# Kernel tuning notes

Measured on AMD Instinct MI355X. Metric: run time of the kernel, lower is better.

Reference implementation:

```python
import jax, jax.numpy as jnp
import numpy as np

K_SIZE = 11  # fixed kernel size in the original module
HALF = K_SIZE // 2  # 5


def setup_inputs() -> dict:
    key = jax.random.key(0)
    N = 16777216  # 2**24 signal length
    inp = jax.random.normal(key, (N,), dtype=jnp.float32)
    scale = jnp.float32(1.0)  # learned scalar parameter (init arg s)
    return {"input": inp, "scale": scale}


def reference(input, scale):
    # Parabolic structuring element: h[k] = -z_k^2 / (4*scale), z_k = -5..5
    z = jnp.linspace(-HALF, HALF, K_SIZE, dtype=jnp.float32)
    h = -(z * z) / (4.0 * scale)  # [11]
    N = input.shape[0]
    # Pad with -inf so boundary windows truncate exactly like the banded matrix.
    padded = jnp.pad(input, (HALF, HALF), constant_values=-jnp.inf)
    # out[i] = max_k padded[i + k] + h[k]  (windowed max-plus / morphological dilation)
    acc = padded[0:N] + h[0]
    for k in range(1, K_SIZE):  # small fixed loop over 11 kernel taps
        acc = jnp.maximum(acc, padded[k:k + N] + h[k])
    return acc
```

## Files before the change

### kernel.cpp

```cpp
#include <hip/hip_runtime.h>
#include <math.h>

#define K_SIZE 11
#define HALF 5
#define BLOCK 256
#define EPT 8
#define TILE (BLOCK*EPT)

__global__ __launch_bounds__(BLOCK) void dilation1d_kernel(
    const float* __restrict__ in, const float* __restrict__ scale_p,
    float* __restrict__ out, int N)
{
    const float inv4s = 1.0f / (4.0f * scale_p[0]);

    const int t = threadIdx.x;
    const int g0 = blockIdx.x * TILE;
    const int base = g0 + t * EPT;
    const int lbase = base - 8;

    float r[24];
    const bool interior = (blockIdx.x != 0) && (blockIdx.x != gridDim.x - 1);
    if (interior) {
        const float4* p = (const float4*)(in + lbase);
        #pragma unroll
        for (int v = 0; v < 6; ++v) {
            float4 f = p[v];
            r[v*4+0] = f.x; r[v*4+1] = f.y; r[v*4+2] = f.z; r[v*4+3] = f.w;
        }
    } else {
        #pragma unroll
        for (int j = 0; j < 24; ++j) {
            int idx = lbase + j;
            r[j] = (idx >= 0 && idx < N) ? in[idx] : -INFINITY;
        }
    }

    float o[EPT];
    #pragma unroll
    for (int u = 0; u < EPT; ++u) {
        float m = -INFINITY;
        #pragma unroll
        for (int k = 0; k < K_SIZE; ++k) {
            const float zk = (float)(k - HALF);
            const float h = -(zk * zk) * inv4s;
            m = fmaxf(m, r[u + k + 3] + h);
        }
        o[u] = m;
    }

    float4* po = (float4*)(out + base);
    po[0] = make_float4(o[0], o[1], o[2], o[3]);
    po[1] = make_float4(o[4], o[5], o[6], o[7]);
}

extern "C" void kernel_launch(void* const* d_in, const int* in_sizes, int n_in,
                              void* d_out, int out_size, void* d_ws, size_t ws_size,
                              hipStream_t stream) {
    const float* in      = (const float*)d_in[0];
    const float* scale_p = (const float*)d_in[1];
    float* out           = (float*)d_out;
    const int N = in_sizes[0];
    const int grid = (N + TILE - 1) / TILE;
    hipLaunchKernelGGL(dilation1d_kernel, dim3(grid), dim3(BLOCK), 0, stream,
                       in, scale_p, out, N);
}
```

Before: 26.60 us.

## Use grid-stride tiles, symmetric tap pairing, and nontemporal output stores

Switches the launch to a fixed grid of at most 2048 blocks that loop over tiles in grid-stride fashion. The tap loop is rewritten to use the symmetry of the parabolic kernel: each symmetric pair is maxed first and a single offset added, which removes about half the adds. Output goes through nontemporal stores, and a guarded tail path is added for partial tiles. The point is to cut launch and tail overhead and ALU work on a memory-bound kernel. In exchange there is less parallelism per launch and possible changes in cache behaviour.

```diff
diff --git a/kernel.cpp b/kernel.cpp
--- a/kernel.cpp
+++ b/kernel.cpp
@@ -6,51 +6,63 @@
 #define BLOCK 256
 #define EPT 8
 #define TILE (BLOCK*EPT)
+#define GRID 2048
+
+typedef float floatx4 __attribute__((ext_vector_type(4)));
 
 __global__ __launch_bounds__(BLOCK) void dilation1d_kernel(
     const float* __restrict__ in, const float* __restrict__ scale_p,
     float* __restrict__ out, int N)
 {
     const float inv4s = 1.0f / (4.0f * scale_p[0]);
+    float h[HALF + 1];
+    #pragma unroll
+    for (int d = 0; d <= HALF; ++d) h[d] = -(float)(d * d) * inv4s;
 
-    const int t = threadIdx.x;
-    const int g0 = blockIdx.x * TILE;
-    const int base = g0 + t * EPT;
-    const int lbase = base - 8;
+    const int ntiles = (N + TILE - 1) / TILE;
+    for (int tile = blockIdx.x; tile < ntiles; tile += gridDim.x) {
+        const int base  = tile * TILE + threadIdx.x * EPT;
+        const int lbase = base - 8;
+        const bool interior = (tile != 0) && (tile != ntiles - 1);
 
-    float r[24];
-    const bool interior = (blockIdx.x != 0) && (blockIdx.x != gridDim.x - 1);
-    if (interior) {
-        const float4* p = (const float4*)(in + lbase);
+        float r[24];
+        if (interior) {
+            const floatx4* p = (const floatx4*)(in + lbase);
+            #pragma unroll
+            for (int v = 0; v < 6; ++v) {
+                floatx4 f = p[v];
+                r[v*4+0] = f.x; r[v*4+1] = f.y; r[v*4+2] = f.z; r[v*4+3] = f.w;
+            }
+        } else {
+            #pragma unroll
+            for (int j = 0; j < 24; ++j) {
+                int idx = lbase + j;
+                r[j] = (idx >= 0 && idx < N) ? in[idx] : -INFINITY;
+            }
+        }
+
+        float o[EPT];
         #pragma unroll
-        for (int v = 0; v < 6; ++v) {
-            float4 f = p[v];
-            r[v*4+0] = f.x; r[v*4+1] = f.y; r[v*4+2] = f.z; r[v*4+3] = f.w;
+        for (int u = 0; u < EPT; ++u) {
+            float m = r[u + 8];
+            #pragma unroll
+            for (int d = 1; d <= HALF; ++d)
+                m = fmaxf(m, fmaxf(r[u + 8 - d], r[u + 8 + d]) + h[d]);
+            o[u] = m;
         }
-    } else {
-        #pragma unroll
-        for (int j = 0; j < 24; ++j) {
-            int idx = lbase + j;
-            r[j] = (idx >= 0 && idx < N) ? in[idx] : -INFINITY;
+
+        if (interior || base + EPT <= N) {
+            floatx4* po = (floatx4*)(out + base);
+            floatx4 v0 = {o[0], o[1], o[2], o[3]};
+            floatx4 v1 = {o[4], o[5], o[6], o[7]};
+            __builtin_nontemporal_store(v0, po);
+            __builtin_nontemporal_store(v1, po + 1);
+        } else {
+            #pragma unroll
+            for (int u = 0; u < EPT; ++u)
+                if (base + u < N) out[base + u] = o[u];
         }
     }
-
-    float o[EPT];
-    #pragma unroll
-    for (int u = 0; u < EPT; ++u) {
-        float m = -INFINITY;
-        #pragma unroll
-        for (int k = 0; k < K_SIZE; ++k) {
-            const float zk = (float)(k - HALF);
-            const float h = -(zk * zk) * inv4s;
-            m = fmaxf(m, r[u + k + 3] + h);
-        }
-        o[u] = m;
-    }
-
-    float4* po = (float4*)(out + base);
-    po[0] = make_float4(o[0], o[1], o[2], o[3]);
-    po[1] = make_float4(o[4], o[5], o[6], o[7]);
 }
 
 extern "C" void kernel_launch(void* const* d_in, const int* in_sizes, int n_in,
@@ -60,7 +72,8 @@
     const float* scale_p = (const float*)d_in[1];
     float* out           = (float*)d_out;
     const int N = in_sizes[0];
-    const int grid = (N + TILE - 1) / TILE;
+    const int ntiles = (N + TILE - 1) / TILE;
+    const int grid = ntiles < GRID ? ntiles : GRID;
     hipLaunchKernelGGL(dilation1d_kernel, dim3(grid), dim3(BLOCK), 0, stream,
                        in, scale_p, out, N);
 }
```

Measured after the change: 28.42 us. 6.9% more time.

## Stage input tile with halo in LDS and exploit symmetric parabolic weights

Applied to the files above, without the earlier changes.

Each block now loads its 2048-element tile plus halo into shared memory with coalesced scalar loads, then each thread reads 20-element windows from LDS for two groups of 4 outputs. This replaces the overlapping per-thread global float4 loads, which fetched 24 values to produce 8 outputs. The tap loop uses the symmetry h[-d]=h[d] to take the max of the pair before adding, which reduces adds. It adds a __syncthreads and LDS traffic, and the global loads become scalar with bounds checks.

```diff
diff --git a/kernel.cpp b/kernel.cpp
--- a/kernel.cpp
+++ b/kernel.cpp
@@ -1,56 +1,70 @@
 #include <hip/hip_runtime.h>
 #include <math.h>
 
-#define K_SIZE 11
 #define HALF 5
 #define BLOCK 256
-#define EPT 8
-#define TILE (BLOCK*EPT)
+#define TILE 2048
+#define SLDS (TILE + 16)
+
+typedef float floatx4 __attribute__((ext_vector_type(4)));
 
 __global__ __launch_bounds__(BLOCK) void dilation1d_kernel(
     const float* __restrict__ in, const float* __restrict__ scale_p,
     float* __restrict__ out, int N)
 {
+    __shared__ float s[SLDS];
     const float inv4s = 1.0f / (4.0f * scale_p[0]);
+    float h[HALF + 1];
+    #pragma unroll
+    for (int d = 0; d <= HALF; ++d) h[d] = -(float)(d * d) * inv4s;
 
-    const int t = threadIdx.x;
+    const int t  = threadIdx.x;
     const int g0 = blockIdx.x * TILE;
-    const int base = g0 + t * EPT;
-    const int lbase = base - 8;
 
-    float r[24];
-    const bool interior = (blockIdx.x != 0) && (blockIdx.x != gridDim.x - 1);
-    if (interior) {
-        const float4* p = (const float4*)(in + lbase);
-        #pragma unroll
-        for (int v = 0; v < 6; ++v) {
-            float4 f = p[v];
-            r[v*4+0] = f.x; r[v*4+1] = f.y; r[v*4+2] = f.z; r[v*4+3] = f.w;
-        }
-    } else {
-        #pragma unroll
-        for (int j = 0; j < 24; ++j) {
-            int idx = lbase + j;
-            r[j] = (idx >= 0 && idx < N) ? in[idx] : -INFINITY;
+    #pragma unroll
+    for (int k = 0; k < 8; ++k) {
+        const int j = t + k * BLOCK;
+        const int idx = g0 - 8 + j;
+        s[j] = ((unsigned)idx < (unsigned)N) ? in[idx] : -INFINITY;
+    }
+    {
+        const int j = t + 8 * BLOCK;
+        if (j < SLDS) {
+            const int idx = g0 - 8 + j;
+            s[j] = ((unsigned)idx < (unsigned)N) ? in[idx] : -INFINITY;
         }
     }
+    __syncthreads();
 
-    float o[EPT];
     #pragma unroll
-    for (int u = 0; u < EPT; ++u) {
-        float m = -INFINITY;
+    for (int grp = 0; grp < 2; ++grp) {
+        const int p = 4 * t + grp * (TILE / 2);
+        float w[20];
+        const floatx4* ps = (const floatx4*)(s + p);
         #pragma unroll
-        for (int k = 0; k < K_SIZE; ++k) {
-            const float zk = (float)(k - HALF);
-            const float h = -(zk * zk) * inv4s;
-            m = fmaxf(m, r[u + k + 3] + h);
+        for (int v = 0; v < 5; ++v) {
+            floatx4 f = ps[v];
+            w[4*v+0] = f.x; w[4*v+1] = f.y; w[4*v+2] = f.z; w[4*v+3] = f.w;
         }
-        o[u] = m;
+        float o[4];
+        #pragma unroll
+        for (int u = 0; u < 4; ++u) {
+            float m = w[u + 8];
+            #pragma unroll
+            for (int d = 1; d <= HALF; ++d)
+                m = fmaxf(m, fmaxf(w[u + 8 - d], w[u + 8 + d]) + h[d]);
+            o[u] = m;
+        }
+        const int go = g0 + p;
+        if (go + 4 <= N) {
+            floatx4 v = {o[0], o[1], o[2], o[3]};
+            *(floatx4*)(out + go) = v;
+        } else {
+            #pragma unroll
+            for (int u = 0; u < 4; ++u)
+                if (go + u < N) out[go + u] = o[u];
+        }
     }
-
-    float4* po = (float4*)(out + base);
-    po[0] = make_float4(o[0], o[1], o[2], o[3]);
-    po[1] = make_float4(o[4], o[5], o[6], o[7]);
 }
 
 extern "C" void kernel_launch(void* const* d_in, const int* in_sizes, int n_in,
```

New measurement: 29.27 us. 1.1x slower.
